# Optimization experiments

Hardware: AMD Instinct MI355X
Metric: run time of the kernel (lower is better)

The kernel has to match this reference:

```python
import jax, jax.numpy as jnp
import numpy as np

B = 16384      # rays
H = 128        # field hidden dim


def setup_inputs() -> dict:
    key = jax.random.key(0)
    ks = jax.random.split(key, 8)
    origins = jax.random.normal(ks[0], (B, 3), dtype=jnp.float32)
    directions = jax.random.normal(ks[1], (B, 3), dtype=jnp.float32)
    directions = directions / jnp.linalg.norm(directions, axis=-1, keepdims=True)
    # Field: simple MLP 3 -> H -> H -> 4 (rgb + sigma)
    W1 = jax.random.normal(ks[2], (3, H), dtype=jnp.float32) * (1.0 / np.sqrt(3.0))
    b1 = jnp.zeros((H,), dtype=jnp.float32)
    W2 = jax.random.normal(ks[3], (H, H), dtype=jnp.float32) * (1.0 / np.sqrt(H))
    b2 = jnp.zeros((H,), dtype=jnp.float32)
    W3 = jax.random.normal(ks[4], (H, 4), dtype=jnp.float32) * (1.0 / np.sqrt(H))
    b3 = jnp.zeros((4,), dtype=jnp.float32)
    return {"origins": origins, "directions": directions,
            "W1": W1, "b1": b1, "W2": W2, "b2": b2, "W3": W3, "b3": b3,
            "near": 2, "far": 6, "num_samples": 64}


def _field(x, W1, b1, W2, b2, W3, b3):
    h = jax.nn.relu(x @ W1 + b1)
    h = jax.nn.relu(h @ W2 + b2)
    return h @ W3 + b3


def reference(origins, directions, W1, b1, W2, b2, W3, b3, near, far, num_samples):
    near = jnp.float32(near)
    far = jnp.float32(far)
    # 1. generate_samples: segment boundaries + midpoints along each ray
    depths = jnp.linspace(near, far, num_samples + 1)            # [S+1]
    midpoints = 0.5 * (depths[:-1] + depths[1:])                 # [S]
    # [B, S, 3] = origin + t * direction
    locs = origins[:, None, :] + midpoints[None, :, None] * directions[:, None, :]
    # 2. evaluate field
    f = _field(locs.reshape(-1, 3), W1, b1, W2, b2, W3, b3)
    f = f.reshape(origins.shape[0], num_samples, 4)
    # NOTE: source overwrites the sigmoid'd colors with raw outputs (faithful)
    colors = f[..., :3]                                          # [B, S, 3]
    sigma = f[..., 3]                                            # [B, S]
    # 3. alpha values
    delta = depths[1:] - depths[:-1]                             # [S]
    alphas = 1.0 - jnp.exp(-sigma * delta[None, :])              # [B, S]
    # 4. alpha compositing (black background)
    ones = jnp.ones_like(alphas[:, :1])
    transmittance = jnp.cumprod(jnp.concatenate([ones, 1.0 - alphas], axis=1), axis=1)[:, :-1]
    weights = alphas * transmittance                             # [B, S]
    radiance = jnp.sum(weights[..., None] * colors, axis=1)      # [B, 3]
    return radiance
```

## Files before the change

### kernel.cpp

```cpp
#include <hip/hip_runtime.h>


typedef _Float16 f16;
typedef __attribute__((ext_vector_type(2))) _Float16 h2v;
typedef __attribute__((ext_vector_type(8))) _Float16 half8;
typedef __attribute__((ext_vector_type(4))) float floatx4;

#define H 128
#define NS 64

static __device__ __forceinline__ h2v pkrtz(float a, float b) {
  return __builtin_bit_cast(h2v, __builtin_amdgcn_cvt_pkrtz(a, b));
}

__global__ void nerf_setup(const float* __restrict__ W2, const float* __restrict__ W3,
                           const float* __restrict__ b2,
                           f16* __restrict__ wsW2, f16* __restrict__ wsW3,
                           f16* __restrict__ wsB2) {
  int t = blockIdx.x * blockDim.x + threadIdx.x;
  if (t < 8192) {
    int j2 = t & 3, lane = (t >> 2) & 63, mt = (t >> 8) & 7, ks = t >> 11;
    int l16 = lane & 15;
    int k = ks * 32 + ((lane >> 4) * 8) + 2 * j2;
    int n = 32 * (l16 >> 2) + mt * 4 + (l16 & 3);
    wsW2[2 * t]     = (f16)W2[k * H + n];
    wsW2[2 * t + 1] = (f16)W2[(k + 1) * H + n];
  } else if (t < 9216) {
    int u = t - 8192;
    int j2 = u & 3, lane = (u >> 2) & 63, ks = u >> 8;
    int c = lane & 15;
    int k3 = 32 * (lane >> 4) + ks * 8 + 2 * j2;
    wsW3[2 * u]     = (c < 4) ? (f16)W3[k3 * 4 + c]       : (f16)0.0f;
    wsW3[2 * u + 1] = (c < 4) ? (f16)W3[(k3 + 1) * 4 + c] : (f16)0.0f;
  } else if (t < 9344) {
    int i = t - 9216;
    wsB2[i] = (f16)b2[i];
  }
}

__global__ __launch_bounds__(256, 3) void nerf_main(
    const float* __restrict__ origins, const float* __restrict__ dirs,
    const float* __restrict__ W1, const float* __restrict__ b1,
    const float* __restrict__ b3,
    const f16* __restrict__ wsW2, const f16* __restrict__ wsW3,
    const f16* __restrict__ wsB2,
    float* __restrict__ out)
{
  __shared__ __align__(16) f16   popd[4][2][H];
  __shared__ __align__(16) float f_lds[2][64][4];

  const int t = threadIdx.x;
  const int w = t >> 6, lane = t & 63, quad = lane >> 4, l16 = lane & 15;
  const int rayw  = w >> 1;
  const int ray   = blockIdx.x * 2 + rayw;
  const int shalf = (w & 1) * 32;
  const float delta = 4.0f / NS;

  {
    const float o0 = origins[ray*3], o1 = origins[ray*3+1], o2 = origins[ray*3+2];
    const float d0 = dirs[ray*3],    d1 = dirs[ray*3+1],    d2 = dirs[ray*3+2];
    const int k0 = lane * 2;
    const float2 wr0 = *(const float2*)&W1[0*H + k0];
    const float2 wr1 = *(const float2*)&W1[1*H + k0];
    const float2 wr2 = *(const float2*)&W1[2*H + k0];
    const float2 bb  = *(const float2*)&b1[k0];
    float poa = fmaf(o2, wr2.x, fmaf(o1, wr1.x, fmaf(o0, wr0.x, bb.x)));
    float pob = fmaf(o2, wr2.y, fmaf(o1, wr1.y, fmaf(o0, wr0.y, bb.y)));
    float pda = fmaf(d2, wr2.x, fmaf(d1, wr1.x, d0 * wr0.x));
    float pdb = fmaf(d2, wr2.y, fmaf(d1, wr1.y, d0 * wr0.y));
    h2v po2; po2[0] = (f16)poa; po2[1] = (f16)pob;
    h2v pd2; pd2[0] = (f16)pda; pd2[1] = (f16)pdb;
    *(h2v*)&popd[w][0][k0] = po2;
    *(h2v*)&popd[w][1][k0] = pd2;
  }

  half8 m8[2];
  #pragma unroll
  for (int tr = 0; tr < 2; ++tr)
    m8[tr] = (half8)(f16)(2.0f + (shalf + tr*16 + l16 + 0.5f) * delta);

  floatx4 acc[8][2];
  #pragma unroll
  for (int mt = 0; mt < 8; ++mt) {
    acc[mt][0] = (floatx4)(0.0f);
    acc[mt][1] = (floatx4)(0.0f);
  }

  const half8* w2f = (const half8*)wsW2;
  const half8 z8 = (half8)(f16)0.0f;
  #pragma unroll
  for (int ks = 0; ks < 4; ++ks) {
    half8 aw[8];
    #pragma unroll
    for (int mt = 0; mt < 8; ++mt) aw[mt] = w2f[(ks*8 + mt)*64 + lane];
    const half8 po8 = *(const half8*)&popd[w][0][ks*32 + quad*8];
    const half8 pd8 = *(const half8*)&popd[w][1][ks*32 + quad*8];
    #pragma unroll
    for (int tr = 0; tr < 2; ++tr) {
      half8 hb = pd8 * m8[tr] + po8;
      hb = __builtin_elementwise_max(hb, z8);
      #pragma unroll
      for (int mt = 0; mt < 8; ++mt)
        acc[mt][tr] = __builtin_amdgcn_mfma_f32_16x16x32_f16(aw[mt], hb, acc[mt][tr], 0, 0, 0);
    }
  }

  h2v bk0[8], bk1[8];
  {
    const uint2* bp = (const uint2*)wsB2;
    #pragma unroll
    for (int mt = 0; mt < 8; ++mt) {
      uint2 u = bp[quad * 8 + mt];
      bk0[mt] = __builtin_bit_cast(h2v, u.x);
      bk1[mt] = __builtin_bit_cast(h2v, u.y);
    }
  }
  const half8* w3f = (const half8*)wsW3;
  half8 w3[4];
  #pragma unroll
  for (int ks = 0; ks < 4; ++ks) w3[ks] = w3f[ks*64 + lane];

  const h2v z2 = (h2v)(f16)0.0f;
  floatx4 acc3[2];
  #pragma unroll
  for (int tr = 0; tr < 2; ++tr) {
    acc3[tr] = (floatx4)(0.0f);
    #pragma unroll
    for (int ks = 0; ks < 4; ++ks) {
      const int mt0 = 2*ks, mt1 = 2*ks + 1;
      h2v c0 = __builtin_elementwise_max((h2v)(pkrtz(acc[mt0][tr][0], acc[mt0][tr][1]) + bk0[mt0]), z2);
      h2v c1 = __builtin_elementwise_max((h2v)(pkrtz(acc[mt0][tr][2], acc[mt0][tr][3]) + bk1[mt0]), z2);
      h2v c2 = __builtin_elementwise_max((h2v)(pkrtz(acc[mt1][tr][0], acc[mt1][tr][1]) + bk0[mt1]), z2);
      h2v c3 = __builtin_elementwise_max((h2v)(pkrtz(acc[mt1][tr][2], acc[mt1][tr][3]) + bk1[mt1]), z2);
      half8 b = { c0[0], c0[1], c1[0], c1[1], c2[0], c2[1], c3[0], c3[1] };
      acc3[tr] = __builtin_amdgcn_mfma_f32_16x16x32_f16(w3[ks], b, acc3[tr], 0, 0, 0);
    }
  }

  if (quad == 0) {
    #pragma unroll
    for (int tr = 0; tr < 2; ++tr) {
      float4 fv;
      fv.x = acc3[tr][0] + b3[0];
      fv.y = acc3[tr][1] + b3[1];
      fv.z = acc3[tr][2] + b3[2];
      fv.w = acc3[tr][3] + b3[3];
      *(float4*)&f_lds[rayw][shalf + tr*16 + l16][0] = fv;
    }
  }
  __syncthreads();

  if (w < 2) {
    const int rray = blockIdx.x * 2 + w;
    const float4 fv = *(const float4*)&f_lds[w][lane][0];
    const float sigma = fv.w;
    const float alpha = 1.0f - __expf(-sigma * delta);
    float S = sigma;
    #pragma unroll
    for (int off = 1; off < 64; off <<= 1) {
      float u = __shfl_up(S, off);
      if (lane >= off) S += u;
    }
    const float T  = __expf(-delta * (S - sigma));
    const float wt = alpha * T;
    float cr = wt * fv.x, cg = wt * fv.y, cb = wt * fv.z;
    #pragma unroll
    for (int off = 32; off > 0; off >>= 1) {
      cr += __shfl_down(cr, off);
      cg += __shfl_down(cg, off);
      cb += __shfl_down(cb, off);
    }
    if (lane == 0) {
      out[rray*3+0] = cr; out[rray*3+1] = cg; out[rray*3+2] = cb;
    }
  }
}

extern "C" void kernel_launch(void* const* d_in, const int* in_sizes, int n_in,
                              void* d_out, int out_size, void* d_ws, size_t ws_size,
                              hipStream_t stream) {
  const float* origins = (const float*)d_in[0];
  const float* dirs    = (const float*)d_in[1];
  const float* W1      = (const float*)d_in[2];
  const float* b1      = (const float*)d_in[3];
  const float* W2      = (const float*)d_in[4];
  const float* b2      = (const float*)d_in[5];
  const float* W3      = (const float*)d_in[6];
  const float* b3      = (const float*)d_in[7];
  float* out = (float*)d_out;

  f16* wsW2 = (f16*)d_ws;
  f16* wsW3 = wsW2 + 16384;
  f16* wsB2 = wsW3 + 2048;

  nerf_setup<<<37, 256, 0, stream>>>(W2, W3, b2, wsW2, wsW3, wsB2);
  nerf_main<<<16384 / 2, 256, 0, stream>>>(
      origins, dirs, W1, b1, b3, wsW2, wsW3, wsB2, out);
}
```

Measured before the change: 121.6 us.

## Split hidden dimension across waves so each wave holds a W2 slice

Each wave now owns 32 of the 128 hidden outputs of layer 2 and processes all 128 samples of the block's two rays, instead of each wave loading the full W2 for 32 samples. The wave's W2 slice, W3 slice and bias are loaded once up front into registers, which cuts per-wave weight traffic by a factor of four. The layer-3 partial outputs from the four waves are summed through LDS before compositing. In exchange it adds an extra barrier, a larger LDS buffer for the partials, and recomputes the layer-1 hidden input for every sample tile.

```diff
diff --git a/kernel.cpp b/kernel.cpp
--- a/kernel.cpp
+++ b/kernel.cpp
@@ -19,17 +19,18 @@
                            f16* __restrict__ wsB2) {
   int t = blockIdx.x * blockDim.x + threadIdx.x;
   if (t < 8192) {
-    int j2 = t & 3, lane = (t >> 2) & 63, mt = (t >> 8) & 7, ks = t >> 11;
+    int j2 = t & 3, lane = (t >> 2) & 63, fid = t >> 8;
+    int mtl = fid & 1, ks = (fid >> 1) & 3, wv = fid >> 3;
     int l16 = lane & 15;
     int k = ks * 32 + ((lane >> 4) * 8) + 2 * j2;
-    int n = 32 * (l16 >> 2) + mt * 4 + (l16 & 3);
+    int n = 32 * wv + (l16 >> 2) * 8 + mtl * 4 + (l16 & 3);
     wsW2[2 * t]     = (f16)W2[k * H + n];
     wsW2[2 * t + 1] = (f16)W2[(k + 1) * H + n];
   } else if (t < 9216) {
     int u = t - 8192;
-    int j2 = u & 3, lane = (u >> 2) & 63, ks = u >> 8;
+    int j2 = u & 3, lane = (u >> 2) & 63, wv = u >> 8;
     int c = lane & 15;
-    int k3 = 32 * (lane >> 4) + ks * 8 + 2 * j2;
+    int k3 = 32 * wv + ((lane >> 4) * 8) + 2 * j2;
     wsW3[2 * u]     = (c < 4) ? (f16)W3[k3 * 4 + c]       : (f16)0.0f;
     wsW3[2 * u + 1] = (c < 4) ? (f16)W3[(k3 + 1) * 4 + c] : (f16)0.0f;
   } else if (t < 9344) {
@@ -46,17 +47,33 @@
     const f16* __restrict__ wsB2,
     float* __restrict__ out)
 {
-  __shared__ __align__(16) f16   popd[4][2][H];
-  __shared__ __align__(16) float f_lds[2][64][4];
+  __shared__ __align__(16) f16   popd[2][2][H];
+  __shared__ __align__(16) float f_lds[4][128][4];
 
   const int t = threadIdx.x;
   const int w = t >> 6, lane = t & 63, quad = lane >> 4, l16 = lane & 15;
-  const int rayw  = w >> 1;
-  const int ray   = blockIdx.x * 2 + rayw;
-  const int shalf = (w & 1) * 32;
   const float delta = 4.0f / NS;
 
+  const half8* w2f = (const half8*)wsW2;
+  half8 aw[4][2];
+  #pragma unroll
+  for (int ks = 0; ks < 4; ++ks)
+    #pragma unroll
+    for (int mtl = 0; mtl < 2; ++mtl)
+      aw[ks][mtl] = w2f[((w * 4 + ks) * 2 + mtl) * 64 + lane];
+  const half8 w3 = ((const half8*)wsW3)[w * 64 + lane];
+  h2v bk[4];
   {
+    uint4 u = *(const uint4*)(wsB2 + 32 * w + quad * 8);
+    bk[0] = __builtin_bit_cast(h2v, u.x);
+    bk[1] = __builtin_bit_cast(h2v, u.y);
+    bk[2] = __builtin_bit_cast(h2v, u.z);
+    bk[3] = __builtin_bit_cast(h2v, u.w);
+  }
+  const float4 b3v = *(const float4*)b3;
+
+  if (w < 2) {
+    const int ray = blockIdx.x * 2 + w;
     const float o0 = origins[ray*3], o1 = origins[ray*3+1], o2 = origins[ray*3+2];
     const float d0 = dirs[ray*3],    d1 = dirs[ray*3+1],    d2 = dirs[ray*3+2];
     const int k0 = lane * 2;
@@ -73,87 +90,65 @@
     *(h2v*)&popd[w][0][k0] = po2;
     *(h2v*)&popd[w][1][k0] = pd2;
   }
+  __syncthreads();
 
-  half8 m8[2];
+  h2v m2[8];
   #pragma unroll
-  for (int tr = 0; tr < 2; ++tr)
-    m8[tr] = (half8)(f16)(2.0f + (shalf + tr*16 + l16 + 0.5f) * delta);
-
-  floatx4 acc[8][2];
-  #pragma unroll
-  for (int mt = 0; mt < 8; ++mt) {
-    acc[mt][0] = (floatx4)(0.0f);
-    acc[mt][1] = (floatx4)(0.0f);
+  for (int nt = 0; nt < 8; ++nt) {
+    const f16 m = (f16)(2.0f + ((nt & 3) * 16 + l16 + 0.5f) * delta);
+    m2[nt][0] = m; m2[nt][1] = m;
   }
 
-  const half8* w2f = (const half8*)wsW2;
-  const half8 z8 = (half8)(f16)0.0f;
+  floatx4 acc[2][8];
+  #pragma unroll
+  for (int nt = 0; nt < 8; ++nt) { acc[0][nt] = (floatx4)(0.0f); acc[1][nt] = (floatx4)(0.0f); }
+
+  const h2v z2 = (h2v)(f16)0.0f;
   #pragma unroll
   for (int ks = 0; ks < 4; ++ks) {
-    half8 aw[8];
+    const half8 poA = *(const half8*)&popd[0][0][ks*32 + quad*8];
+    const half8 pdA = *(const half8*)&popd[0][1][ks*32 + quad*8];
+    const half8 poB = *(const half8*)&popd[1][0][ks*32 + quad*8];
+    const half8 pdB = *(const half8*)&popd[1][1][ks*32 + quad*8];
     #pragma unroll
-    for (int mt = 0; mt < 8; ++mt) aw[mt] = w2f[(ks*8 + mt)*64 + lane];
-    const half8 po8 = *(const half8*)&popd[w][0][ks*32 + quad*8];
-    const half8 pd8 = *(const half8*)&popd[w][1][ks*32 + quad*8];
-    #pragma unroll
-    for (int tr = 0; tr < 2; ++tr) {
-      half8 hb = pd8 * m8[tr] + po8;
-      hb = __builtin_elementwise_max(hb, z8);
+    for (int nt = 0; nt < 8; ++nt) {
+      union { half8 v; h2v p[4]; } P, O, Hb;
+      P.v = (nt < 4) ? pdA : pdB;
+      O.v = (nt < 4) ? poA : poB;
       #pragma unroll
-      for (int mt = 0; mt < 8; ++mt)
-        acc[mt][tr] = __builtin_amdgcn_mfma_f32_16x16x32_f16(aw[mt], hb, acc[mt][tr], 0, 0, 0);
+      for (int p2 = 0; p2 < 4; ++p2)
+        Hb.p[p2] = __builtin_elementwise_max((h2v)(P.p[p2] * m2[nt] + O.p[p2]), z2);
+      acc[0][nt] = __builtin_amdgcn_mfma_f32_16x16x32_f16(aw[ks][0], Hb.v, acc[0][nt], 0, 0, 0);
+      acc[1][nt] = __builtin_amdgcn_mfma_f32_16x16x32_f16(aw[ks][1], Hb.v, acc[1][nt], 0, 0, 0);
     }
   }
 
-  h2v bk0[8], bk1[8];
-  {
-    const uint2* bp = (const uint2*)wsB2;
-    #pragma unroll
-    for (int mt = 0; mt < 8; ++mt) {
-      uint2 u = bp[quad * 8 + mt];
-      bk0[mt] = __builtin_bit_cast(h2v, u.x);
-      bk1[mt] = __builtin_bit_cast(h2v, u.y);
-    }
-  }
-  const half8* w3f = (const half8*)wsW3;
-  half8 w3[4];
   #pragma unroll
-  for (int ks = 0; ks < 4; ++ks) w3[ks] = w3f[ks*64 + lane];
-
-  const h2v z2 = (h2v)(f16)0.0f;
-  floatx4 acc3[2];
-  #pragma unroll
-  for (int tr = 0; tr < 2; ++tr) {
-    acc3[tr] = (floatx4)(0.0f);
-    #pragma unroll
-    for (int ks = 0; ks < 4; ++ks) {
-      const int mt0 = 2*ks, mt1 = 2*ks + 1;
-      h2v c0 = __builtin_elementwise_max((h2v)(pkrtz(acc[mt0][tr][0], acc[mt0][tr][1]) + bk0[mt0]), z2);
-      h2v c1 = __builtin_elementwise_max((h2v)(pkrtz(acc[mt0][tr][2], acc[mt0][tr][3]) + bk1[mt0]), z2);
-      h2v c2 = __builtin_elementwise_max((h2v)(pkrtz(acc[mt1][tr][0], acc[mt1][tr][1]) + bk0[mt1]), z2);
-      h2v c3 = __builtin_elementwise_max((h2v)(pkrtz(acc[mt1][tr][2], acc[mt1][tr][3]) + bk1[mt1]), z2);
-      half8 b = { c0[0], c0[1], c1[0], c1[1], c2[0], c2[1], c3[0], c3[1] };
-      acc3[tr] = __builtin_amdgcn_mfma_f32_16x16x32_f16(w3[ks], b, acc3[tr], 0, 0, 0);
-    }
-  }
-
-  if (quad == 0) {
-    #pragma unroll
-    for (int tr = 0; tr < 2; ++tr) {
-      float4 fv;
-      fv.x = acc3[tr][0] + b3[0];
-      fv.y = acc3[tr][1] + b3[1];
-      fv.z = acc3[tr][2] + b3[2];
-      fv.w = acc3[tr][3] + b3[3];
-      *(float4*)&f_lds[rayw][shalf + tr*16 + l16][0] = fv;
+  for (int nt = 0; nt < 8; ++nt) {
+    h2v c0 = __builtin_elementwise_max((h2v)(pkrtz(acc[0][nt][0], acc[0][nt][1]) + bk[0]), z2);
+    h2v c1 = __builtin_elementwise_max((h2v)(pkrtz(acc[0][nt][2], acc[0][nt][3]) + bk[1]), z2);
+    h2v c2 = __builtin_elementwise_max((h2v)(pkrtz(acc[1][nt][0], acc[1][nt][1]) + bk[2]), z2);
+    h2v c3 = __builtin_elementwise_max((h2v)(pkrtz(acc[1][nt][2], acc[1][nt][3]) + bk[3]), z2);
+    half8 b = { c0[0], c0[1], c1[0], c1[1], c2[0], c2[1], c3[0], c3[1] };
+    floatx4 d = __builtin_amdgcn_mfma_f32_16x16x32_f16(w3, b, (floatx4)(0.0f), 0, 0, 0);
+    if (quad == 0) {
+      float4 fv; fv.x = d[0]; fv.y = d[1]; fv.z = d[2]; fv.w = d[3];
+      *(float4*)&f_lds[w][nt*16 + l16][0] = fv;
     }
   }
   __syncthreads();
 
   if (w < 2) {
-    const int rray = blockIdx.x * 2 + w;
-    const float4 fv = *(const float4*)&f_lds[w][lane][0];
-    const float sigma = fv.w;
+    const int p = w * 64 + lane;
+    const float4 s0 = *(const float4*)&f_lds[0][p][0];
+    const float4 s1 = *(const float4*)&f_lds[1][p][0];
+    const float4 s2 = *(const float4*)&f_lds[2][p][0];
+    const float4 s3 = *(const float4*)&f_lds[3][p][0];
+    const float fr = s0.x + s1.x + s2.x + s3.x + b3v.x;
+    const float fg = s0.y + s1.y + s2.y + s3.y + b3v.y;
+    const float fb = s0.z + s1.z + s2.z + s3.z + b3v.z;
+    const float sigma = s0.w + s1.w + s2.w + s3.w + b3v.w;
+
     const float alpha = 1.0f - __expf(-sigma * delta);
     float S = sigma;
     #pragma unroll
@@ -163,7 +158,7 @@
     }
     const float T  = __expf(-delta * (S - sigma));
     const float wt = alpha * T;
-    float cr = wt * fv.x, cg = wt * fv.y, cb = wt * fv.z;
+    float cr = wt * fr, cg = wt * fg, cb = wt * fb;
     #pragma unroll
     for (int off = 32; off > 0; off >>= 1) {
       cr += __shfl_down(cr, off);
@@ -171,7 +166,8 @@
       cb += __shfl_down(cb, off);
     }
     if (lane == 0) {
-      out[rray*3+0] = cr; out[rray*3+1] = cg; out[rray*3+2] = cb;
+      const int ray = blockIdx.x * 2 + w;
+      out[ray*3+0] = cr; out[ray*3+1] = cg; out[ray*3+2] = cb;
     }
   }
 }
```

New measurement: 117.2 us. -3.6%, faster.
